# Optimization experiments

Hardware: AMD Instinct MI355X
Metric: run time of the kernel (lower is better)

Reference implementation:

```python
import jax, jax.numpy as jnp
import numpy as np

B, SRC = 32, 1024
SEQ_LEN, CONTEXT_LEN, D_MODEL, VOCAB = 128, 5, 512, 32000


def setup_inputs() -> dict:
    key = jax.random.key(0)
    k1, k2, k3, k4, k5, k6 = jax.random.split(key, 6)
    x = jax.random.randint(k1, (B, SRC), 0, VOCAB, dtype=jnp.int64 if jax.config.jax_enable_x64 else jnp.int32)
    yc = jax.random.randint(k2, (B, SEQ_LEN * CONTEXT_LEN), 0, VOCAB, dtype=x.dtype)
    F_emb = jax.random.normal(k3, (VOCAB, D_MODEL), dtype=jnp.float32) * 0.02
    G_emb = jax.random.normal(k4, (VOCAB, D_MODEL), dtype=jnp.float32) * 0.02
    fan_in = CONTEXT_LEN * D_MODEL
    P_w = jax.random.uniform(k5, (fan_in, D_MODEL), dtype=jnp.float32,
                             minval=-1.0, maxval=1.0) * (fan_in ** -0.5)
    P_b = jnp.zeros((D_MODEL,), dtype=jnp.float32)
    return {"x": x, "yc": yc, "F_emb": F_emb, "G_emb": G_emb, "P_w": P_w, "P_b": P_b}


def reference(x, yc, F_emb, G_emb, P_w, P_b):
    # padding mask from source tokens: 1.0 where token == 0
    mask = (x == 0).astype(jnp.float32)                      # [B, SRC]
    xe = F_emb[x]                                            # [B, SRC, D]
    yce = G_emb[yc].reshape(-1, SEQ_LEN, CONTEXT_LEN * D_MODEL)  # [B, SEQ, C*D]
    py = jnp.einsum('bsk,kd->bsd', yce, P_w) + P_b           # Dense P(y): [B, SEQ, D]
    a = jnp.einsum('bxd,bsd->bxs', xe, py)                   # [B, SRC, SEQ]
    a = a + mask[:, :, None] * -1e9                          # mask padded source rows
    a = jnp.transpose(a, (0, 2, 1))                          # [B, SEQ, SRC]
    a = jax.nn.softmax(a, axis=-1)
    out = jnp.einsum('bsx,bxd->bsd', a, xe)                  # [B, SEQ, D]
    return (out, a)
```

## Files before the change

### kernel.cpp

```cpp
#include <hip/hip_runtime.h>
#include <hip/hip_bf16.h>
#include <stdint.h>

#define BATCH 32
#define SRCN 1024
#define SEQL 128
#define CTXN 5
#define DMOD 512

typedef __attribute__((ext_vector_type(8))) short short8;
typedef __attribute__((ext_vector_type(4))) float floatx4;

typedef __attribute__((address_space(3))) void lds_t;
typedef __attribute__((address_space(1))) void glb_t;

__device__ __forceinline__ void gload_lds16(const void* g, void* l) {
    __builtin_amdgcn_global_load_lds((const glb_t*)g, (lds_t*)l, 16, 0, 0);
}

__device__ __forceinline__ ushort f2b(float f) {
    __hip_bfloat16 h = __float2bfloat16(f);
    return *reinterpret_cast<ushort*>(&h);
}

#define LSLOT(m, sg) ((((m) << 3) | ((sg) ^ ((m) & 7))) << 3)

#define PSTR 69

__global__ __launch_bounds__(256) void k_gather(
    const int* __restrict__ yc, const float* __restrict__ G,
    ushort* __restrict__ yce,
    const float* __restrict__ Pw, ushort* __restrict__ Pwt,
    const int* __restrict__ x, const float* __restrict__ F,
    ushort* __restrict__ xe, ushort* __restrict__ xet)
{
    __shared__ __align__(16) char smem[17664];
    const int tid = threadIdx.x;
    const int bid = blockIdx.x;
    if (bid < 4096) {
        int* toks = (int*)smem;
        const int r = bid;
        const int b = r >> 7, s = r & 127;
        if (tid < CTXN) toks[tid] = yc[b * (SEQL * CTXN) + s * CTXN + tid];
        __syncthreads();
        for (int i = tid; i < 640; i += 256) {
            const int c = i >> 7;
            const int tok = toks[c];
            const float4 v = *(const float4*)(G + (size_t)tok * DMOD + (i & 127) * 4);
            ushort4 o;
            o.x = f2b(v.x); o.y = f2b(v.y); o.z = f2b(v.z); o.w = f2b(v.w);
            *(ushort4*)(yce + (size_t)r * 2560 + i * 4) = o;
        }
    } else if (bid < 4416) {
        float* tf = (float*)smem;
        const int id = bid - 4096;
        const int k0 = (id % 40) * 64, n0 = (id / 40) * 64;
        #pragma unroll
        for (int it = 0; it < 4; ++it) {
            const int c = tid + it * 256;
            const int kr = c >> 4, c4 = c & 15;
            const float4 v = *(const float4*)(Pw + (size_t)(k0 + kr) * DMOD + n0 + c4 * 4);
            tf[kr * PSTR + c4 * 4 + 0] = v.x; tf[kr * PSTR + c4 * 4 + 1] = v.y;
            tf[kr * PSTR + c4 * 4 + 2] = v.z; tf[kr * PSTR + c4 * 4 + 3] = v.w;
        }
        __syncthreads();
        #pragma unroll
        for (int it = 0; it < 2; ++it) {
            const int c = tid + it * 256;
            const int n = c >> 3, seg = c & 7;
            ushort4 o0, o1;
            o0.x = f2b(tf[(seg * 8 + 0) * PSTR + n]); o0.y = f2b(tf[(seg * 8 + 1) * PSTR + n]);
            o0.z = f2b(tf[(seg * 8 + 2) * PSTR + n]); o0.w = f2b(tf[(seg * 8 + 3) * PSTR + n]);
            o1.x = f2b(tf[(seg * 8 + 4) * PSTR + n]); o1.y = f2b(tf[(seg * 8 + 5) * PSTR + n]);
            o1.z = f2b(tf[(seg * 8 + 6) * PSTR + n]); o1.w = f2b(tf[(seg * 8 + 7) * PSTR + n]);
            ushort* dst = Pwt + (size_t)(n0 + n) * 2560 + k0 + seg * 8;
            *(ushort4*)dst = o0; *(ushort4*)(dst + 4) = o1;
        }
    } else {
        ushort* t = (ushort*)smem;
        int* toks = (int*)(smem + 16384);
        const int id = bid - 4416;
        const int z = id >> 6;
        const int rem = id & 63;
        const int x0 = (rem & 7) * 128, d0 = (rem >> 3) * 64;
        if (tid < 128) toks[tid] = x[z * SRCN + x0 + tid];
        __syncthreads();
        #pragma unroll
        for (int it = 0; it < 8; ++it) {
            const int c = tid + it * 256;
            const int row = c >> 4, seg = c & 15;
            const int tok = toks[row];
            const float4 v = *(const float4*)(F + (size_t)tok * DMOD + d0 + seg * 4);
            ushort4 o;
            o.x = f2b(v.x); o.y = f2b(v.y); o.z = f2b(v.z); o.w = f2b(v.w);
            const int sg2 = seg ^ ((row >> 3) & 15);
            *(ushort4*)&t[row * 64 + sg2 * 4] = o;
            *(ushort4*)(xe + (size_t)(z * SRCN + x0 + row) * DMOD + d0 + seg * 4) = o;
        }
        __syncthreads();
        #pragma unroll
        for (int it = 0; it < 4; ++it) {
            const int c = tid + it * 256;
            const int xs = c & 15, d = c >> 4;
            const int sbase = ((d >> 2) ^ xs) * 4 + (d & 3);
            short8 o;
            #pragma unroll
            for (int r = 0; r < 8; ++r)
                o[r] = (short)t[(xs * 8 + r) * 64 + sbase];
            *(short8*)(xet + (size_t)(z * DMOD + d0 + d) * SRCN + x0 + xs * 8) = o;
        }
    }
}

__global__ __launch_bounds__(256) void k_gemm_py(
    const ushort* __restrict__ yce, const ushort* __restrict__ pwt,
    float* __restrict__ part)
{
    __shared__ ushort As[16 * 512];
    __shared__ ushort Bs[8 * 512];
    const int f = blockIdx.x;
    const int ks  = f >> 8;
    const int idx = f & 255;
    const int mlo = idx & 7;
    const int n   = (idx >> 3) & 7;
    const int mhi = idx >> 6;
    const int m = mlo | (mhi << 3);
    const int tid = threadIdx.x;
    const int w = tid >> 6, lane = tid & 63;
    const int l15 = lane & 15, q = lane >> 4;
    const int wm = w >> 1, wn = w & 1;
    const int m0 = m * 128, n0 = n * 64, koff = ks * 1280;

    const int sr = lane >> 3;
    const int ssg = ((lane & 7) ^ sr) * 8;

    const ushort* Abase = yce + (size_t)(m0 + sr) * 2560 + koff + ssg;
    const ushort* Bbase = pwt + (size_t)(n0 + sr) * 2560 + koff + ssg;

    floatx4 acc[4][2];
    #pragma unroll
    for (int mi = 0; mi < 4; ++mi)
        #pragma unroll
        for (int ni = 0; ni < 2; ++ni)
            acc[mi][ni] = (floatx4){0.f, 0.f, 0.f, 0.f};

    for (int kk = 0; kk < 1280; kk += 64) {
        __syncthreads();
        #pragma unroll
        for (int i = 0; i < 4; ++i) {
            const int cc = w * 4 + i;
            gload_lds16(Abase + (size_t)(cc * 8) * 2560 + kk, (void*)(As + cc * 512));
        }
        #pragma unroll
        for (int i = 0; i < 2; ++i) {
            const int cc = w * 2 + i;
            gload_lds16(Bbase + (size_t)(cc * 8) * 2560 + kk, (void*)(Bs + cc * 512));
        }
        __syncthreads();
        #pragma unroll
        for (int s2 = 0; s2 < 2; ++s2) {
            const int sg = s2 * 4 + q;
            short8 af[4], bf[2];
            #pragma unroll
            for (int mi = 0; mi < 4; ++mi)
                af[mi] = *(const short8*)(As + LSLOT(wm * 64 + mi * 16 + l15, sg));
            #pragma unroll
            for (int ni = 0; ni < 2; ++ni)
                bf[ni] = *(const short8*)(Bs + LSLOT(wn * 32 + ni * 16 + l15, sg));
            #pragma unroll
            for (int mi = 0; mi < 4; ++mi)
                #pragma unroll
                for (int ni = 0; ni < 2; ++ni)
                    acc[mi][ni] = __builtin_amdgcn_mfma_f32_16x16x32_bf16(
                        af[mi], bf[ni], acc[mi][ni], 0, 0, 0);
        }
    }

    float* dst = part + (size_t)ks * (4096LL * DMOD);
    #pragma unroll
    for (int ni = 0; ni < 2; ++ni) {
        const int col = n0 + wn * 32 + ni * 16 + l15;
        #pragma unroll
        for (int mi = 0; mi < 4; ++mi) {
            const int row0 = m0 + wm * 64 + mi * 16 + q * 4;
            #pragma unroll
            for (int r = 0; r < 4; ++r)
                dst[(size_t)(row0 + r) * DMOD + col] = acc[mi][ni][r];
        }
    }
}

__global__ __launch_bounds__(256) void k_red2(
    const float* __restrict__ part, const float* __restrict__ Pb,
    ushort* __restrict__ py)
{
    const long long SL = 4096LL * DMOD;
    const int i = blockIdx.x * 256 + threadIdx.x;
    const float4 a = *(const float4*)(part + (size_t)i * 4);
    const float4 b = *(const float4*)(part + SL + (size_t)i * 4);
    const float4 bias = *(const float4*)(Pb + ((i * 4) & 511));
    ushort4 o;
    o.x = f2b(a.x + b.x + bias.x);
    o.y = f2b(a.y + b.y + bias.y);
    o.z = f2b(a.z + b.z + bias.z);
    o.w = f2b(a.w + b.w + bias.w);
    *(ushort4*)(py + (size_t)i * 4) = o;
}

__global__ __launch_bounds__(256) void k_gemm_sc(
    const ushort* __restrict__ py, const int* __restrict__ x,
    const ushort* __restrict__ xe, float* __restrict__ a_out)
{
    __shared__ ushort As[16 * 512];
    __shared__ ushort Bs[8 * 512];
    const int f = blockIdx.x;
    const int g = f >> 3;
    const int b = ((g & 3) << 3) | (f & 7);
    const int n = g >> 2;
    const int tid = threadIdx.x;
    const int w = tid >> 6, lane = tid & 63;
    const int l15 = lane & 15, q = lane >> 4;
    const int wm = w >> 1, wn = w & 1;
    const int n0 = n * 64;

    const int sr = lane >> 3;
    const int ssg = ((lane & 7) ^ sr) * 8;

    const ushort* Abase = py + (size_t)(b * SEQL + sr) * DMOD + ssg;
    const ushort* Bbase = xe + (size_t)(b * SRCN + n0 + sr) * DMOD + ssg;

    floatx4 acc[4][2];
    #pragma unroll
    for (int mi = 0; mi < 4; ++mi)
        #pragma unroll
        for (int ni = 0; ni < 2; ++ni)
            acc[mi][ni] = (floatx4){0.f, 0.f, 0.f, 0.f};

    for (int kk = 0; kk < DMOD; kk += 64) {
        __syncthreads();
        #pragma unroll
        for (int i = 0; i < 4; ++i) {
            const int cc = w * 4 + i;
            gload_lds16(Abase + (size_t)(cc * 8) * DMOD + kk, (void*)(As + cc * 512));
        }
        #pragma unroll
        for (int i = 0; i < 2; ++i) {
            const int cc = w * 2 + i;
            gload_lds16(Bbase + (size_t)(cc * 8) * DMOD + kk, (void*)(Bs + cc * 512));
        }
        __syncthreads();
        #pragma unroll
        for (int s2 = 0; s2 < 2; ++s2) {
            const int sg = s2 * 4 + q;
            short8 af[4], bf[2];
            #pragma unroll
            for (int mi = 0; mi < 4; ++mi)
                af[mi] = *(const short8*)(As + LSLOT(wm * 64 + mi * 16 + l15, sg));
            #pragma unroll
            for (int ni = 0; ni < 2; ++ni)
                bf[ni] = *(const short8*)(Bs + LSLOT(wn * 32 + ni * 16 + l15, sg));
            #pragma unroll
            for (int mi = 0; mi < 4; ++mi)
                #pragma unroll
                for (int ni = 0; ni < 2; ++ni)
                    acc[mi][ni] = __builtin_amdgcn_mfma_f32_16x16x32_bf16(
                        af[mi], bf[ni], acc[mi][ni], 0, 0, 0);
        }
    }

    #pragma unroll
    for (int ni = 0; ni < 2; ++ni) {
        const int col = n0 + wn * 32 + ni * 16 + l15;
        const float msk = (x[b * SRCN + col] == 0) ? -1e9f : 0.0f;
        #pragma unroll
        for (int mi = 0; mi < 4; ++mi) {
            const int row0 = wm * 64 + mi * 16 + q * 4;
            #pragma unroll
            for (int r = 0; r < 4; ++r)
                a_out[((size_t)b * SEQL + row0 + r) * SRCN + col] = acc[mi][ni][r] + msk;
        }
    }
}

__global__ __launch_bounds__(256) void k_softmax(
    float* __restrict__ a, ushort* __restrict__ abf)
{
    const int row = blockIdx.x;
    float* p = a + (size_t)row * SRCN;
    ushort* pb = abf + (size_t)row * SRCN;
    const int tid = threadIdx.x;
    const int wave = tid >> 6, lane = tid & 63;

    float4 v = *(const float4*)(p + tid * 4);

    float mx = fmaxf(fmaxf(v.x, v.y), fmaxf(v.z, v.w));
    #pragma unroll
    for (int off = 32; off > 0; off >>= 1)
        mx = fmaxf(mx, __shfl_down(mx, off, 64));
    __shared__ float redm[4];
    if (lane == 0) redm[wave] = mx;
    __syncthreads();
    mx = fmaxf(fmaxf(redm[0], redm[1]), fmaxf(redm[2], redm[3]));

    const float e0 = __expf(v.x - mx);
    const float e1 = __expf(v.y - mx);
    const float e2 = __expf(v.z - mx);
    const float e3 = __expf(v.w - mx);

    float sm = e0 + e1 + e2 + e3;
    #pragma unroll
    for (int off = 32; off > 0; off >>= 1)
        sm += __shfl_down(sm, off, 64);
    __shared__ float reds[4];
    if (lane == 0) reds[wave] = sm;
    __syncthreads();
    sm = reds[0] + reds[1] + reds[2] + reds[3];

    const float inv = 1.0f / sm;
    float4 o;
    o.x = e0 * inv; o.y = e1 * inv; o.z = e2 * inv; o.w = e3 * inv;
    *(float4*)(p + tid * 4) = o;
    ushort4 ob;
    ob.x = f2b(o.x); ob.y = f2b(o.y); ob.z = f2b(o.z); ob.w = f2b(o.w);
    *(ushort4*)(pb + tid * 4) = ob;
}

__global__ __launch_bounds__(256) void k_gemm_out(
    const ushort* __restrict__ abf, const ushort* __restrict__ xet,
    float* __restrict__ outp)
{
    __shared__ ushort As[2 * 8 * 512];
    __shared__ ushort Bs[2 * 8 * 512];
    const int f = blockIdx.x;
    const int g = f >> 3;
    const int b = ((g & 3) << 3) | (f & 7);
    const int h = g >> 2;
    const int m = h & 1, n = h >> 1;
    const int tid = threadIdx.x;
    const int w = tid >> 6, lane = tid & 63;
    const int l15 = lane & 15, q = lane >> 4;
    const int wm = w >> 1, wn = w & 1;
    const int m0 = m * 64, n0 = n * 64;

    const int sr = lane >> 3;
    const int ssg = ((lane & 7) ^ sr) * 8;

    const ushort* Abase = abf + (size_t)(b * SEQL + m0 + sr) * SRCN + ssg;
    const ushort* Bbase = xet + (size_t)(b * DMOD + n0 + sr) * SRCN + ssg;

    floatx4 acc[2][2];
    #pragma unroll
    for (int mi = 0; mi < 2; ++mi)
        #pragma unroll
        for (int ni = 0; ni < 2; ++ni)
            acc[mi][ni] = (floatx4){0.f, 0.f, 0.f, 0.f};

    for (int kk = 0; kk < SRCN; kk += 128) {
        __syncthreads();
        #pragma unroll
        for (int sub = 0; sub < 2; ++sub) {
            #pragma unroll
            for (int i = 0; i < 2; ++i) {
                const int cc = w * 2 + i;
                gload_lds16(Abase + (size_t)(cc * 8) * SRCN + kk + sub * 64,
                            (void*)(As + sub * 4096 + cc * 512));
                gload_lds16(Bbase + (size_t)(cc * 8) * SRCN + kk + sub * 64,
                            (void*)(Bs + sub * 4096 + cc * 512));
            }
        }
        __syncthreads();
        #pragma unroll
        for (int sub = 0; sub < 2; ++sub) {
            #pragma unroll
            for (int s2 = 0; s2 < 2; ++s2) {
                const int sg = s2 * 4 + q;
                short8 af[2], bf[2];
                #pragma unroll
                for (int mi = 0; mi < 2; ++mi)
                    af[mi] = *(const short8*)(As + sub * 4096 + LSLOT(wm * 32 + mi * 16 + l15, sg));
                #pragma unroll
                for (int ni = 0; ni < 2; ++ni)
                    bf[ni] = *(const short8*)(Bs + sub * 4096 + LSLOT(wn * 32 + ni * 16 + l15, sg));
                #pragma unroll
                for (int mi = 0; mi < 2; ++mi)
                    #pragma unroll
                    for (int ni = 0; ni < 2; ++ni)
                        acc[mi][ni] = __builtin_amdgcn_mfma_f32_16x16x32_bf16(
                            af[mi], bf[ni], acc[mi][ni], 0, 0, 0);
            }
        }
    }

    #pragma unroll
    for (int ni = 0; ni < 2; ++ni) {
        const int col = n0 + wn * 32 + ni * 16 + l15;
        #pragma unroll
        for (int mi = 0; mi < 2; ++mi) {
            const int row0 = m0 + wm * 32 + mi * 16 + q * 4;
            #pragma unroll
            for (int r = 0; r < 4; ++r)
                outp[((size_t)b * SEQL + row0 + r) * DMOD + col] = acc[mi][ni][r];
        }
    }
}

extern "C" void kernel_launch(void* const* d_in, const int* in_sizes, int n_in,
                              void* d_out, int out_size, void* d_ws, size_t ws_size,
                              hipStream_t stream)
{
    const int*   x    = (const int*)d_in[0];
    const int*   yc   = (const int*)d_in[1];
    const float* Femb = (const float*)d_in[2];
    const float* Gemb = (const float*)d_in[3];
    const float* Pw   = (const float*)d_in[4];
    const float* Pb   = (const float*)d_in[5];

    float* out_p = (float*)d_out;
    float* a_p   = out_p + (size_t)BATCH * SEQL * DMOD;

    char* ws = (char*)d_ws;
    ushort* yce  = (ushort*)(ws);
    ushort* abf  = (ushort*)(ws);
    ushort* pwt  = (ushort*)(ws + 20971520);
    ushort* xe   = (ushort*)(ws + 23592960);
    ushort* xet  = (ushort*)(ws + 57147392);
    float*  part = (float*) (ws + 90701824);
    ushort* py   = (ushort*)(ws + 107479040);

    dim3 blk(256);
    k_gather<<<dim3(6464), blk, 0, stream>>>(yc, Gemb, yce, Pw, pwt, x, Femb, xe, xet);

    k_gemm_py<<<dim3(512), blk, 0, stream>>>(yce, pwt, part);
    k_red2<<<dim3(2048), blk, 0, stream>>>(part, Pb, py);

    k_gemm_sc<<<dim3(512), blk, 0, stream>>>(py, x, xe, a_p);
    k_softmax<<<dim3(4096), blk, 0, stream>>>(a_p, abf);
    k_gemm_out<<<dim3(512), blk, 0, stream>>>(abf, xet, out_p);
}
```

Baseline: 220.4 us.

## Double-buffer LDS tiles in the three GEMM kernels to overlap loads with MFMA

Converts the projection, score and output GEMM loops into double-buffered pipelines. The next K-slice is issued with global_load_lds into the alternate LDS buffer while MFMAs run on the current one, with one barrier per iteration instead of two. The goal is to hide global-memory latency behind compute. In exchange it doubles LDS use in two kernels, which may lower occupancy, and its correctness depends on the async global-to-LDS loads completing before the barrier.

```diff
diff --git a/kernel.cpp b/kernel.cpp
--- a/kernel.cpp
+++ b/kernel.cpp
@@ -116,8 +116,8 @@
     const ushort* __restrict__ yce, const ushort* __restrict__ pwt,
     float* __restrict__ part)
 {
-    __shared__ ushort As[16 * 512];
-    __shared__ ushort Bs[8 * 512];
+    __shared__ ushort As[2 * 8192];
+    __shared__ ushort Bs[2 * 4096];
     const int f = blockIdx.x;
     const int ks  = f >> 8;
     const int idx = f & 255;
@@ -144,29 +144,34 @@
         for (int ni = 0; ni < 2; ++ni)
             acc[mi][ni] = (floatx4){0.f, 0.f, 0.f, 0.f};
 
-    for (int kk = 0; kk < 1280; kk += 64) {
-        __syncthreads();
-        #pragma unroll
-        for (int i = 0; i < 4; ++i) {
-            const int cc = w * 4 + i;
-            gload_lds16(Abase + (size_t)(cc * 8) * 2560 + kk, (void*)(As + cc * 512));
-        }
-        #pragma unroll
-        for (int i = 0; i < 2; ++i) {
-            const int cc = w * 2 + i;
-            gload_lds16(Bbase + (size_t)(cc * 8) * 2560 + kk, (void*)(Bs + cc * 512));
-        }
-        __syncthreads();
+#define STAGE_PY(buf, kk) do { \
+    _Pragma("unroll") \
+    for (int i = 0; i < 4; ++i) { \
+        const int cc = w * 4 + i; \
+        gload_lds16(Abase + (size_t)(cc * 8) * 2560 + (kk), (void*)(As + (buf) * 8192 + cc * 512)); \
+    } \
+    _Pragma("unroll") \
+    for (int i = 0; i < 2; ++i) { \
+        const int cc = w * 2 + i; \
+        gload_lds16(Bbase + (size_t)(cc * 8) * 2560 + (kk), (void*)(Bs + (buf) * 4096 + cc * 512)); \
+    } } while (0)
+
+    STAGE_PY(0, 0);
+    __syncthreads();
+    #pragma unroll
+    for (int t = 0; t < 20; ++t) {
+        const int cur = t & 1;
+        if (t < 19) STAGE_PY(cur ^ 1, (t + 1) * 64);
         #pragma unroll
         for (int s2 = 0; s2 < 2; ++s2) {
             const int sg = s2 * 4 + q;
             short8 af[4], bf[2];
             #pragma unroll
             for (int mi = 0; mi < 4; ++mi)
-                af[mi] = *(const short8*)(As + LSLOT(wm * 64 + mi * 16 + l15, sg));
+                af[mi] = *(const short8*)(As + cur * 8192 + LSLOT(wm * 64 + mi * 16 + l15, sg));
             #pragma unroll
             for (int ni = 0; ni < 2; ++ni)
-                bf[ni] = *(const short8*)(Bs + LSLOT(wn * 32 + ni * 16 + l15, sg));
+                bf[ni] = *(const short8*)(Bs + cur * 4096 + LSLOT(wn * 32 + ni * 16 + l15, sg));
             #pragma unroll
             for (int mi = 0; mi < 4; ++mi)
                 #pragma unroll
@@ -174,7 +179,9 @@
                     acc[mi][ni] = __builtin_amdgcn_mfma_f32_16x16x32_bf16(
                         af[mi], bf[ni], acc[mi][ni], 0, 0, 0);
         }
-    }
+        __syncthreads();
+    }
+#undef STAGE_PY
 
     float* dst = part + (size_t)ks * (4096LL * DMOD);
     #pragma unroll
@@ -211,8 +218,8 @@
     const ushort* __restrict__ py, const int* __restrict__ x,
     const ushort* __restrict__ xe, float* __restrict__ a_out)
 {
-    __shared__ ushort As[16 * 512];
-    __shared__ ushort Bs[8 * 512];
+    __shared__ ushort As[2 * 8192];
+    __shared__ ushort Bs[2 * 4096];
     const int f = blockIdx.x;
     const int g = f >> 3;
     const int b = ((g & 3) << 3) | (f & 7);
@@ -236,29 +243,34 @@
         for (int ni = 0; ni < 2; ++ni)
             acc[mi][ni] = (floatx4){0.f, 0.f, 0.f, 0.f};
 
-    for (int kk = 0; kk < DMOD; kk += 64) {
-        __syncthreads();
-        #pragma unroll
-        for (int i = 0; i < 4; ++i) {
-            const int cc = w * 4 + i;
-            gload_lds16(Abase + (size_t)(cc * 8) * DMOD + kk, (void*)(As + cc * 512));
-        }
-        #pragma unroll
-        for (int i = 0; i < 2; ++i) {
-            const int cc = w * 2 + i;
-            gload_lds16(Bbase + (size_t)(cc * 8) * DMOD + kk, (void*)(Bs + cc * 512));
-        }
-        __syncthreads();
+#define STAGE_SC(buf, kk) do { \
+    _Pragma("unroll") \
+    for (int i = 0; i < 4; ++i) { \
+        const int cc = w * 4 + i; \
+        gload_lds16(Abase + (size_t)(cc * 8) * DMOD + (kk), (void*)(As + (buf) * 8192 + cc * 512)); \
+    } \
+    _Pragma("unroll") \
+    for (int i = 0; i < 2; ++i) { \
+        const int cc = w * 2 + i; \
+        gload_lds16(Bbase + (size_t)(cc * 8) * DMOD + (kk), (void*)(Bs + (buf) * 4096 + cc * 512)); \
+    } } while (0)
+
+    STAGE_SC(0, 0);
+    __syncthreads();
+    #pragma unroll
+    for (int t = 0; t < 8; ++t) {
+        const int cur = t & 1;
+        if (t < 7) STAGE_SC(cur ^ 1, (t + 1) * 64);
         #pragma unroll
         for (int s2 = 0; s2 < 2; ++s2) {
             const int sg = s2 * 4 + q;
             short8 af[4], bf[2];
             #pragma unroll
             for (int mi = 0; mi < 4; ++mi)
-                af[mi] = *(const short8*)(As + LSLOT(wm * 64 + mi * 16 + l15, sg));
+                af[mi] = *(const short8*)(As + cur * 8192 + LSLOT(wm * 64 + mi * 16 + l15, sg));
             #pragma unroll
             for (int ni = 0; ni < 2; ++ni)
-                bf[ni] = *(const short8*)(Bs + LSLOT(wn * 32 + ni * 16 + l15, sg));
+                bf[ni] = *(const short8*)(Bs + cur * 4096 + LSLOT(wn * 32 + ni * 16 + l15, sg));
             #pragma unroll
             for (int mi = 0; mi < 4; ++mi)
                 #pragma unroll
@@ -266,7 +278,9 @@
                     acc[mi][ni] = __builtin_amdgcn_mfma_f32_16x16x32_bf16(
                         af[mi], bf[ni], acc[mi][ni], 0, 0, 0);
         }
-    }
+        __syncthreads();
+    }
+#undef STAGE_SC
 
     #pragma unroll
     for (int ni = 0; ni < 2; ++ni) {
@@ -329,8 +343,8 @@
     const ushort* __restrict__ abf, const ushort* __restrict__ xet,
     float* __restrict__ outp)
 {
-    __shared__ ushort As[2 * 8 * 512];
-    __shared__ ushort Bs[2 * 8 * 512];
+    __shared__ ushort As[2 * 4096];
+    __shared__ ushort Bs[2 * 4096];
     const int f = blockIdx.x;
     const int g = f >> 3;
     const int b = ((g & 3) << 3) | (f & 7);
@@ -355,41 +369,40 @@
         for (int ni = 0; ni < 2; ++ni)
             acc[mi][ni] = (floatx4){0.f, 0.f, 0.f, 0.f};
 
-    for (int kk = 0; kk < SRCN; kk += 128) {
-        __syncthreads();
-        #pragma unroll
-        for (int sub = 0; sub < 2; ++sub) {
-            #pragma unroll
-            for (int i = 0; i < 2; ++i) {
-                const int cc = w * 2 + i;
-                gload_lds16(Abase + (size_t)(cc * 8) * SRCN + kk + sub * 64,
-                            (void*)(As + sub * 4096 + cc * 512));
-                gload_lds16(Bbase + (size_t)(cc * 8) * SRCN + kk + sub * 64,
-                            (void*)(Bs + sub * 4096 + cc * 512));
-            }
-        }
-        __syncthreads();
-        #pragma unroll
-        for (int sub = 0; sub < 2; ++sub) {
-            #pragma unroll
-            for (int s2 = 0; s2 < 2; ++s2) {
-                const int sg = s2 * 4 + q;
-                short8 af[2], bf[2];
-                #pragma unroll
-                for (int mi = 0; mi < 2; ++mi)
-                    af[mi] = *(const short8*)(As + sub * 4096 + LSLOT(wm * 32 + mi * 16 + l15, sg));
+#define STAGE_O(buf, kk) do { \
+    _Pragma("unroll") \
+    for (int i = 0; i < 2; ++i) { \
+        const int cc = w * 2 + i; \
+        gload_lds16(Abase + (size_t)(cc * 8) * SRCN + (kk), (void*)(As + (buf) * 4096 + cc * 512)); \
+        gload_lds16(Bbase + (size_t)(cc * 8) * SRCN + (kk), (void*)(Bs + (buf) * 4096 + cc * 512)); \
+    } } while (0)
+
+    STAGE_O(0, 0);
+    __syncthreads();
+    #pragma unroll
+    for (int t = 0; t < 16; ++t) {
+        const int cur = t & 1;
+        if (t < 15) STAGE_O(cur ^ 1, (t + 1) * 64);
+        #pragma unroll
+        for (int s2 = 0; s2 < 2; ++s2) {
+            const int sg = s2 * 4 + q;
+            short8 af[2], bf[2];
+            #pragma unroll
+            for (int mi = 0; mi < 2; ++mi)
+                af[mi] = *(const short8*)(As + cur * 4096 + LSLOT(wm * 32 + mi * 16 + l15, sg));
+            #pragma unroll
+            for (int ni = 0; ni < 2; ++ni)
+                bf[ni] = *(const short8*)(Bs + cur * 4096 + LSLOT(wn * 32 + ni * 16 + l15, sg));
+            #pragma unroll
+            for (int mi = 0; mi < 2; ++mi)
                 #pragma unroll
                 for (int ni = 0; ni < 2; ++ni)
-                    bf[ni] = *(const short8*)(Bs + sub * 4096 + LSLOT(wn * 32 + ni * 16 + l15, sg));
-                #pragma unroll
-                for (int mi = 0; mi < 2; ++mi)
-                    #pragma unroll
-                    for (int ni = 0; ni < 2; ++ni)
-                        acc[mi][ni] = __builtin_amdgcn_mfma_f32_16x16x32_bf16(
-                            af[mi], bf[ni], acc[mi][ni], 0, 0, 0);
-            }
-        }
-    }
+                    acc[mi][ni] = __builtin_amdgcn_mfma_f32_16x16x32_bf16(
+                        af[mi], bf[ni], acc[mi][ni], 0, 0, 0);
+        }
+        __syncthreads();
+    }
+#undef STAGE_O
 
     #pragma unroll
     for (int ni = 0; ni < 2; ++ni) {
```

Result: slower. 231.5 us (+5.0%).
